# Performance work log

Hardware: AMD Instinct MI355X
Metric: run time of the kernel (lower is better)

The kernel has to match this reference:

```python
import jax, jax.numpy as jnp
from jax import lax
import numpy as np

EPS = 1e-8

def squash(x, axis=-1):
    sq = jnp.sum(x * x, axis=axis, keepdims=True)
    return sq / (1.0 + sq) * x / (jnp.sqrt(sq) + EPS)

def conv1d(x, w, b):
    # x: [B, Cin, L], w: [Cout, Cin, K]
    y = lax.conv_general_dilated(x, w, (1,), 'VALID',
                                 dimension_numbers=('NCH', 'OIH', 'NCH'))
    return y + b[None, :, None]

def setup_inputs() -> dict:
    key = jax.random.key(0)
    ks = jax.random.split(key, 6)
    B = 4096
    x = jax.random.normal(ks[0], (B, 50, 128), dtype=jnp.float32)
    conv1_w = jax.random.normal(ks[1], (50, 128, 9), dtype=jnp.float32) * (1.0 / np.sqrt(128 * 9))
    conv1_b = jnp.zeros((50,), dtype=jnp.float32)
    pconv_w = jax.random.normal(ks[2], (64, 42, 3), dtype=jnp.float32) * (1.0 / np.sqrt(42 * 3))
    pconv_b = jnp.zeros((64,), dtype=jnp.float32)
    W = 0.01 * jax.random.normal(ks[3], (5, 384, 16, 8), dtype=jnp.float32)
    return {"x": x, "conv1_w": conv1_w, "conv1_b": conv1_b,
            "pconv_w": pconv_w, "pconv_b": pconv_b, "W": W}

def reference(x, conv1_w, conv1_b, pconv_w, pconv_b, W):
    B = x.shape[0]
    NUM_ROUTING = 3
    # conv + relu: [B,50,128] -> [B,128,50] -> conv -> [B,50,42] -> permute -> [B,42,50]
    h = conv1d(jnp.transpose(x, (0, 2, 1)), conv1_w, conv1_b)
    h = jnp.transpose(jax.nn.relu(h), (0, 2, 1))  # [B,42,50]
    # primary caps: conv1d -> [B,64,48] -> reshape [B,384,8] -> squash
    p = conv1d(h, pconv_w, pconv_b)
    u = squash(p.reshape(B, -1, 8), axis=-1)  # [B,384,8]
    # u_hat[b,o,c,d] = W[o,c,d,i] * u[b,c,i]
    u_hat = jnp.einsum('ocdi,bci->bocd', W, u)  # [B,5,384,16]
    tu = lax.stop_gradient(u_hat)
    b = jnp.zeros((B, 5, 384, 1), dtype=u_hat.dtype)
    for _ in range(NUM_ROUTING - 1):
        c = jax.nn.softmax(b, axis=1)            # [B,5,384,1]
        s = jnp.sum(c * tu, axis=2)              # [B,5,16]
        v = squash(s)                            # [B,5,16]
        uv = jnp.einsum('bocd,bod->boc', tu, v)[..., None]
        b = b + uv
    c = jax.nn.softmax(b, axis=1)
    s = jnp.sum(c * u_hat, axis=2)
    v = squash(s)  # [B,5,16]
    return v
```

## Files before the change

kernel.cpp:

```cpp
#include <hip/hip_runtime.h>
#include <hip/hip_bf16.h>

typedef unsigned short ushort_t;
typedef _Float16 h2 __attribute__((ext_vector_type(2)));
typedef _Float16 half4_t __attribute__((ext_vector_type(4)));
typedef _Float16 half8_t __attribute__((ext_vector_type(8)));
typedef float f32x4 __attribute__((ext_vector_type(4)));
#define EPSQ 1e-8f

__device__ __forceinline__ float fdot2f(h2 a, h2 b, float c) {
#if __has_builtin(__builtin_amdgcn_fdot2)
  return __builtin_amdgcn_fdot2(a, b, c, false);
#else
  return fmaf((float)a.x, (float)b.x, fmaf((float)a.y, (float)b.y, c));
#endif
}
__device__ __forceinline__ h2 bc_h2(unsigned int v) { return __builtin_bit_cast(h2, v); }
__device__ __forceinline__ unsigned int bc_u32(h2 v) { return __builtin_bit_cast(unsigned int, v); }
__device__ __forceinline__ ushort_t bc_u16(_Float16 v) { return __builtin_bit_cast(ushort_t, v); }


__global__ __launch_bounds__(256) void k0_prep(
    const float* __restrict__ w1, const float* __restrict__ pw,
    const float* __restrict__ Wf,
    _Float16* __restrict__ wc16, _Float16* __restrict__ pwB16,
    _Float16* __restrict__ Wh)
{
  int i = blockIdx.x * 256 + threadIdx.x;
  if (i < 73728) {
    int c  = i / 8192;
    int r  = i % 8192;
    int co = r >> 7;
    int k  = r & 127;
    wc16[i] = (co < 50) ? (_Float16)w1[co*1152 + k*9 + c] : (_Float16)0.f;
  }
  if (i < 10240) {
    int co2 = i / 160, kk = i % 160;
    int k = kk / 48, ci = kk % 48;
    float v = (k < 3 && ci < 42) ? pw[co2*126 + ci*3 + k] : 0.f;
    pwB16[i] = (_Float16)v;
  }
  Wh[i] = (_Float16)Wf[i];
}

__global__ __launch_bounds__(256) void k12_mfma(
    const float* __restrict__ x, const float* __restrict__ b1,
    const float* __restrict__ b2, const _Float16* __restrict__ wc16,
    const _Float16* __restrict__ pwB16, ushort_t* __restrict__ u16)
{
  __shared__ float smem[19728];
  _Float16* xh   = (_Float16*)smem;
  _Float16* hr16 = (_Float16*)smem;
  _Float16* pB   = (_Float16*)smem + 8736;
  float*    pbuf = smem + 9744;

  const int tid   = threadIdx.x;
  const int w     = tid >> 6;
  const int lane  = tid & 63;
  const int lc    = lane & 15;
  const int qd    = lane >> 4;
  const int gbase = blockIdx.x * 3;

  for (int j = tid; j < 4800; j += 256) {
    int g = j / 1600, r = j - g*1600;
    int p = r >> 5, q = r & 31;
    int bb = gbase + g; if (bb > 4095) bb = 4095;
    float4 v = *(const float4*)(x + bb*6400 + p*128 + q*4);
    half4_t hv = {(_Float16)v.x, (_Float16)v.y, (_Float16)v.z, (_Float16)v.w};
    *(half4_t*)(xh + g*6800 + p*136 + q*4) = hv;
  }
  {
    const uint4* wg = (const uint4*)wc16;
    uint4* dst = (uint4*)(xh + 20400);
#pragma unroll
    for (int it = 0; it < 4; ++it) {
      int f = it*256 + tid;
      dst[(f >> 4)*17 + (f & 15)] = wg[f];
    }
  }

  const _Float16* abase[2];
#pragma unroll
  for (int tm = 0; tm < 2; ++tm) {
    int m = 32*w + 16*tm + lc;
    if (m > 125) m = 125;
    int g = m / 42, l = m - g*42;
    abase[tm] = xh + g*6800 + l*136 + qd*8;
  }

  f32x4 acc[2][4];
#pragma unroll
  for (int tm = 0; tm < 2; ++tm)
#pragma unroll
    for (int tn = 0; tn < 4; ++tn)
      acc[tm][tn] = (f32x4){0.f, 0.f, 0.f, 0.f};

  __syncthreads();

  uint4 pf[4];
  for (int c = 0; c < 9; ++c) {
    if (c < 8) {
      const uint4* wg = (const uint4*)wc16 + (c + 1)*1024;
#pragma unroll
      for (int it = 0; it < 4; ++it) pf[it] = wg[it*256 + tid];
    }
    const _Float16* Bb = xh + 20400 + (c & 1)*8704;
    const _Float16* a0 = abase[0] + c*136;
    const _Float16* a1 = abase[1] + c*136;
#pragma unroll
    for (int kk = 0; kk < 128; kk += 32) {
      half8_t av0 = *(const half8_t*)(a0 + kk);
      half8_t av1 = *(const half8_t*)(a1 + kk);
#pragma unroll
      for (int tn = 0; tn < 4; ++tn) {
        half8_t bv = *(const half8_t*)(Bb + (16*tn + lc)*136 + qd*8 + kk);
        acc[0][tn] = __builtin_amdgcn_mfma_f32_16x16x32_f16(av0, bv, acc[0][tn], 0, 0, 0);
        acc[1][tn] = __builtin_amdgcn_mfma_f32_16x16x32_f16(av1, bv, acc[1][tn], 0, 0, 0);
      }
    }
    __syncthreads();
    if (c < 8) {
      uint4* dst = (uint4*)(xh + 20400 + ((c + 1) & 1)*8704);
#pragma unroll
      for (int it = 0; it < 4; ++it) {
        int f = it*256 + tid;
        dst[(f >> 4)*17 + (f & 15)] = pf[it];
      }
      __syncthreads();
    }
  }

  for (int j = tid; j < 4368; j += 256) smem[j] = 0.f;
  {
    const uint4* pg = (const uint4*)pwB16;
    uint4* dst = (uint4*)pB;
    for (int f = tid; f < 1280; f += 256) {
      int row = f / 20, cc = f - row*20;
      dst[row*21 + cc] = pg[f];
    }
  }
  __syncthreads();

#pragma unroll
  for (int tm = 0; tm < 2; ++tm) {
    int mb = 32*w + 16*tm + 4*qd;
#pragma unroll
    for (int tn = 0; tn < 4; ++tn) {
      int co = 16*tn + lc;
      if (co < 50) {
        float bias = b1[co];
#pragma unroll
        for (int r = 0; r < 4; ++r) {
          int m = mb + r;
          if (m < 126) {
            int g = m / 42, l = m - g*42;
            hr16[g*2912 + co*56 + l] = (_Float16)fmaxf(acc[tm][tn][r] + bias, 0.f);
          }
        }
      }
    }
  }
  __syncthreads();

  f32x4 acc2[3][4];
#pragma unroll
  for (int tm = 0; tm < 3; ++tm)
#pragma unroll
    for (int tn = 0; tn < 4; ++tn)
      acc2[tm][tn] = (f32x4){0.f, 0.f, 0.f, 0.f};

#pragma unroll
  for (int kc = 0; kc < 5; ++kc) {
    int kk0 = kc*32 + qd*8;
    int k   = (kk0 >= 144) ? 3 : (kk0 >= 96) ? 2 : (kk0 >= 48) ? 1 : 0;
    int ci0 = kk0 - k*48;
    half8_t bv[4];
#pragma unroll
    for (int tn = 0; tn < 4; ++tn)
      bv[tn] = *(const half8_t*)(pB + (16*tn + lc)*168 + kk0);
#pragma unroll
    for (int tm = 0; tm < 3; ++tm) {
      int T = w + 4*tm; int Tc = (T < 9) ? T : 8;
      int g = Tc/3, l2 = (Tc - g*3)*16 + lc;
      half8_t av = *(const half8_t*)(hr16 + g*2912 + (l2 + k)*56 + ci0);
#pragma unroll
      for (int tn = 0; tn < 4; ++tn)
        acc2[tm][tn] = __builtin_amdgcn_mfma_f32_16x16x32_f16(av, bv[tn], acc2[tm][tn], 0, 0, 0);
    }
  }

#pragma unroll
  for (int tm = 0; tm < 3; ++tm) {
    int T = w + 4*tm;
    if (T < 9) {
      int g = T/3, l2b = (T - g*3)*16;
#pragma unroll
      for (int tn = 0; tn < 4; ++tn) {
        int co2 = 16*tn + lc;
        float bias2 = b2[co2];
#pragma unroll
        for (int r = 0; r < 4; ++r) {
          int l2 = l2b + 4*qd + r;
          pbuf[g*3328 + co2*52 + l2] = acc2[tm][tn][r] + bias2;
        }
      }
    }
  }
  __syncthreads();

  for (int idx = tid; idx < 1152; idx += 256) {
    int g = idx / 384, cap = idx - g*384;
    int bb = gbase + g;
    if (bb < 4096) {
      int co2 = cap / 6, gg = cap - co2*6;
      const float* pp = pbuf + g*3328 + co2*52 + gg*8;
      float4 a0 = *(const float4*)pp;
      float4 a1 = *(const float4*)(pp + 4);
      float sq = a0.x*a0.x + a0.y*a0.y + a0.z*a0.z + a0.w*a0.w
               + a1.x*a1.x + a1.y*a1.y + a1.z*a1.z + a1.w*a1.w;
      float sc = sq / ((1.f + sq) * (sqrtf(sq) + EPSQ));
      h2 p0 = {(_Float16)(a0.x*sc), (_Float16)(a0.y*sc)};
      h2 p1 = {(_Float16)(a0.z*sc), (_Float16)(a0.w*sc)};
      h2 p2 = {(_Float16)(a1.x*sc), (_Float16)(a1.y*sc)};
      h2 p3 = {(_Float16)(a1.z*sc), (_Float16)(a1.w*sc)};
      *(uint4*)(u16 + ((size_t)bb*384 + cap)*8) =
          make_uint4(bc_u32(p0), bc_u32(p1), bc_u32(p2), bc_u32(p3));
    }
  }
}

__global__ __launch_bounds__(384) void k3_route(
    const ushort_t* __restrict__ u16, const _Float16* __restrict__ Wh,
    float* __restrict__ out)
{
  __shared__ __align__(16) ushort_t uh16[80][416];
  __shared__ __align__(16) ushort_t coc16[5][416];
  __shared__ __align__(16) ushort_t svh16[80];
  __shared__ float sv[80];
  __shared__ float ff[5];

  const int t  = threadIdx.x;
  const int b  = blockIdx.x;
  const int q  = t / 96;
  const int jc = t - q*96;
  const int ch = q*104 + jc;

  uint4 uu0 = *(const uint4*)(u16 + ((size_t)b*384 + t)*8);
  h2 ua0[4] = {bc_h2(uu0.x), bc_h2(uu0.y), bc_h2(uu0.z), bc_h2(uu0.w)};

  h2 uhreg[40];
#pragma unroll
  for (int o = 0; o < 5; ++o) {
    const uint4* wp = (const uint4*)(Wh + ((size_t)o*384 + t)*128);
#pragma unroll
    for (int dd = 0; dd < 8; ++dd) {
      uint4 w0 = wp[2*dd], w1 = wp[2*dd + 1];
      float s00 = fdot2f(bc_h2(w0.x), ua0[0], fdot2f(bc_h2(w0.y), ua0[1],
                  fdot2f(bc_h2(w0.z), ua0[2], fdot2f(bc_h2(w0.w), ua0[3], 0.f))));
      float s10 = fdot2f(bc_h2(w1.x), ua0[0], fdot2f(bc_h2(w1.y), ua0[1],
                  fdot2f(bc_h2(w1.z), ua0[2], fdot2f(bc_h2(w1.w), ua0[3], 0.f))));
      _Float16 f00 = (_Float16)s00, f10 = (_Float16)s10;
      uh16[o*16 + 2*dd][ch]     = bc_u16(f00);
      uh16[o*16 + 2*dd + 1][ch] = bc_u16(f10);
      uhreg[o*8 + dd] = (h2){f00, f10};
    }
  }

  float lg[5] = {0.f, 0.f, 0.f, 0.f, 0.f};

  for (int it = 0; it < 3; ++it) {
    {
      float m = fmaxf(fmaxf(fmaxf(lg[0],lg[1]),fmaxf(lg[2],lg[3])),lg[4]);
      float e[5]; float Z = 0.f;
#pragma unroll
      for (int o = 0; o < 5; ++o) { e[o] = __expf(lg[o]-m); Z += e[o]; }
      float inv = 1.f / Z;
#pragma unroll
      for (int o = 0; o < 5; ++o) {
        _Float16 hc = (_Float16)(e[o]*inv);
        coc16[o][ch] = bc_u16(hc);
      }
    }
    __syncthreads();

    if (t < 320) {
      int od = t >> 2, qq = t & 3, o = od >> 4;
      const uint4* ua = (const uint4*)&uh16[od][qq*104];
      const uint4* ca = (const uint4*)&coc16[o][qq*104];
      float sum = 0.f;
#pragma unroll
      for (int j = 0; j < 12; ++j) {
        uint4 uv = ua[j];
        uint4 cv = ca[j];
        sum = fdot2f(bc_h2(uv.x), bc_h2(cv.x), sum);
        sum = fdot2f(bc_h2(uv.y), bc_h2(cv.y), sum);
        sum = fdot2f(bc_h2(uv.z), bc_h2(cv.z), sum);
        sum = fdot2f(bc_h2(uv.w), bc_h2(cv.w), sum);
      }
      sum += __shfl_xor(sum, 1);
      sum += __shfl_xor(sum, 2);
      if (qq == 0) sv[od] = sum;
    }
    __syncthreads();

    if (t < 5) {
      int o = t;
      float sq = 0.f;
#pragma unroll
      for (int d = 0; d < 16; ++d) { float v = sv[o*16+d]; sq = fmaf(v, v, sq); }
      float f = sq / ((1.f + sq) * (sqrtf(sq) + EPSQ));
      ff[o] = f;
      if (it < 2) {
#pragma unroll
        for (int d = 0; d < 16; ++d) {
          _Float16 hf = (_Float16)(sv[o*16+d] * f);
          svh16[o*16+d] = bc_u16(hf);
        }
      }
    }
    __syncthreads();

    if (it == 2) {
      if (t < 80) {
        out[(size_t)b*80 + t] = sv[t] * ff[t >> 4];
      }
    } else {
#pragma unroll
      for (int o = 0; o < 5; ++o) {
        uint4 s0 = *(const uint4*)&svh16[o*16];
        uint4 s1 = *(const uint4*)&svh16[o*16 + 8];
        float dv = 0.f;
        dv = fdot2f(uhreg[o*8+0], bc_h2(s0.x), dv);
        dv = fdot2f(uhreg[o*8+1], bc_h2(s0.y), dv);
        dv = fdot2f(uhreg[o*8+2], bc_h2(s0.z), dv);
        dv = fdot2f(uhreg[o*8+3], bc_h2(s0.w), dv);
        dv = fdot2f(uhreg[o*8+4], bc_h2(s1.x), dv);
        dv = fdot2f(uhreg[o*8+5], bc_h2(s1.y), dv);
        dv = fdot2f(uhreg[o*8+6], bc_h2(s1.z), dv);
        dv = fdot2f(uhreg[o*8+7], bc_h2(s1.w), dv);
        lg[o] += dv;
      }
    }
  }
}

extern "C" void kernel_launch(void* const* d_in, const int* in_sizes, int n_in,
                              void* d_out, int out_size, void* d_ws, size_t ws_size,
                              hipStream_t stream) {
  const float* x  = (const float*)d_in[0];
  const float* w1 = (const float*)d_in[1];
  const float* b1 = (const float*)d_in[2];
  const float* pw = (const float*)d_in[3];
  const float* b2 = (const float*)d_in[4];
  const float* Wf = (const float*)d_in[5];
  float* out = (float*)d_out;
  char* ws = (char*)d_ws;

  _Float16* wc16  = (_Float16*)(ws);
  _Float16* pwB16 = (_Float16*)(ws + 147456);
  _Float16* Wh    = (_Float16*)(ws + 167936);
  ushort_t* u16   = (ushort_t*)(ws + 659456);

  k0_prep<<<960, 256, 0, stream>>>(w1, pw, Wf, wc16, pwB16, Wh);
  k12_mfma<<<1366, 256, 0, stream>>>(x, b1, b2, wc16, pwB16, u16);
  k3_route<<<4096, 384, 0, stream>>>(u16, Wh, out);
}
```

Before: 517.8 us.

## Replace shared-memory routing reduction with wave DPP reductions and coalesced W layout

The routing kernel no longer stages u_hat and coupling coefficients in a large shared array. Each thread keeps its u_hat in registers, multiplies by the softmax coefficients, and reduces across the wave with DPP row shifts and xor shuffles. Per-wave partials are written to a small shared buffer, and the squash norm is computed with shuffles instead of a single-thread loop. The W tensor is also reordered in the prep kernel so that consecutive threads load contiguous 16-byte chunks, which coalesces the global reads. Together these cut LDS footprint and barriers, but add many cross-lane reduction ops (16 values times 5 capsules per iteration).

```diff
diff --git a/kernel.cpp b/kernel.cpp
--- a/kernel.cpp
+++ b/kernel.cpp
@@ -19,12 +19,18 @@
 __device__ __forceinline__ unsigned int bc_u32(h2 v) { return __builtin_bit_cast(unsigned int, v); }
 __device__ __forceinline__ ushort_t bc_u16(_Float16 v) { return __builtin_bit_cast(ushort_t, v); }
 
+template<int CTRL>
+__device__ __forceinline__ float dpp_addf(float x) {
+  int y = __builtin_amdgcn_update_dpp(0, __builtin_bit_cast(int, x), CTRL, 0xf, 0xf, false);
+  return x + __builtin_bit_cast(float, y);
+}
+
 
 __global__ __launch_bounds__(256) void k0_prep(
     const float* __restrict__ w1, const float* __restrict__ pw,
     const float* __restrict__ Wf,
     _Float16* __restrict__ wc16, _Float16* __restrict__ pwB16,
-    _Float16* __restrict__ Wh)
+    _Float16* __restrict__ Whs)
 {
   int i = blockIdx.x * 256 + threadIdx.x;
   if (i < 73728) {
@@ -40,7 +46,15 @@
     float v = (k < 3 && ci < 42) ? pw[co2*126 + ci*3 + k] : 0.f;
     pwB16[i] = (_Float16)v;
   }
-  Wh[i] = (_Float16)Wf[i];
+  {
+    int i8 = i & 7;
+    int r  = i >> 3;
+    int d  = r & 15;
+    int rc = r >> 4;
+    int c  = rc % 384;
+    int o  = rc / 384;
+    Whs[(((o*16 + d)*384) + c)*8 + i8] = (_Float16)Wf[i];
+  }
 }
 
 __global__ __launch_bounds__(256) void k12_mfma(
@@ -229,102 +243,96 @@
   }
 }
 
-__global__ __launch_bounds__(384) void k3_route(
-    const ushort_t* __restrict__ u16, const _Float16* __restrict__ Wh,
+__global__ __launch_bounds__(384, 4) void k3_route(
+    const ushort_t* __restrict__ u16, const _Float16* __restrict__ Whs,
     float* __restrict__ out)
 {
-  __shared__ __align__(16) ushort_t uh16[80][416];
-  __shared__ __align__(16) ushort_t coc16[5][416];
+  __shared__ __align__(16) float part[6][80];
   __shared__ __align__(16) ushort_t svh16[80];
-  __shared__ float sv[80];
-  __shared__ float ff[5];
-
-  const int t  = threadIdx.x;
-  const int b  = blockIdx.x;
-  const int q  = t / 96;
-  const int jc = t - q*96;
-  const int ch = q*104 + jc;
+
+  const int t    = threadIdx.x;
+  const int b    = blockIdx.x;
+  const int w    = t >> 6;
+  const int lane = t & 63;
 
   uint4 uu0 = *(const uint4*)(u16 + ((size_t)b*384 + t)*8);
   h2 ua0[4] = {bc_h2(uu0.x), bc_h2(uu0.y), bc_h2(uu0.z), bc_h2(uu0.w)};
 
   h2 uhreg[40];
+  const uint4* wb = (const uint4*)Whs;
 #pragma unroll
   for (int o = 0; o < 5; ++o) {
-    const uint4* wp = (const uint4*)(Wh + ((size_t)o*384 + t)*128);
+    const uint4* wp = wb + (size_t)(o*16)*384 + t;
 #pragma unroll
     for (int dd = 0; dd < 8; ++dd) {
-      uint4 w0 = wp[2*dd], w1 = wp[2*dd + 1];
+      uint4 w0 = wp[(size_t)(2*dd)*384];
+      uint4 w1 = wp[(size_t)(2*dd + 1)*384];
       float s00 = fdot2f(bc_h2(w0.x), ua0[0], fdot2f(bc_h2(w0.y), ua0[1],
                   fdot2f(bc_h2(w0.z), ua0[2], fdot2f(bc_h2(w0.w), ua0[3], 0.f))));
       float s10 = fdot2f(bc_h2(w1.x), ua0[0], fdot2f(bc_h2(w1.y), ua0[1],
                   fdot2f(bc_h2(w1.z), ua0[2], fdot2f(bc_h2(w1.w), ua0[3], 0.f))));
-      _Float16 f00 = (_Float16)s00, f10 = (_Float16)s10;
-      uh16[o*16 + 2*dd][ch]     = bc_u16(f00);
-      uh16[o*16 + 2*dd + 1][ch] = bc_u16(f10);
-      uhreg[o*8 + dd] = (h2){f00, f10};
+      uhreg[o*8 + dd] = (h2){(_Float16)s00, (_Float16)s10};
     }
   }
 
   float lg[5] = {0.f, 0.f, 0.f, 0.f, 0.f};
 
   for (int it = 0; it < 3; ++it) {
+    float co[5];
     {
       float m = fmaxf(fmaxf(fmaxf(lg[0],lg[1]),fmaxf(lg[2],lg[3])),lg[4]);
-      float e[5]; float Z = 0.f;
-#pragma unroll
-      for (int o = 0; o < 5; ++o) { e[o] = __expf(lg[o]-m); Z += e[o]; }
+      float Z = 0.f;
+#pragma unroll
+      for (int o = 0; o < 5; ++o) { co[o] = __expf(lg[o]-m); Z += co[o]; }
       float inv = 1.f / Z;
 #pragma unroll
-      for (int o = 0; o < 5; ++o) {
-        _Float16 hc = (_Float16)(e[o]*inv);
-        coc16[o][ch] = bc_u16(hc);
+      for (int o = 0; o < 5; ++o) co[o] *= inv;
+    }
+
+#pragma unroll
+    for (int o = 0; o < 5; ++o) {
+      float pr[16];
+#pragma unroll
+      for (int dd = 0; dd < 8; ++dd) {
+        h2 uh = uhreg[o*8 + dd];
+        pr[2*dd]     = co[o] * (float)uh.x;
+        pr[2*dd + 1] = co[o] * (float)uh.y;
+      }
+#pragma unroll
+      for (int j = 0; j < 16; ++j) {
+        float v = pr[j];
+        v = dpp_addf<0x121>(v);
+        v = dpp_addf<0x122>(v);
+        v = dpp_addf<0x124>(v);
+        v = dpp_addf<0x128>(v);
+        v += __shfl_xor(v, 16);
+        v += __shfl_xor(v, 32);
+        pr[j] = v;
+      }
+#pragma unroll
+      for (int j = 0; j < 8; ++j) {
+        if (lane == o*8 + j) {
+          *(float2*)&part[w][o*16 + 2*j] = make_float2(pr[2*j], pr[2*j + 1]);
+        }
       }
     }
     __syncthreads();
 
-    if (t < 320) {
-      int od = t >> 2, qq = t & 3, o = od >> 4;
-      const uint4* ua = (const uint4*)&uh16[od][qq*104];
-      const uint4* ca = (const uint4*)&coc16[o][qq*104];
-      float sum = 0.f;
-#pragma unroll
-      for (int j = 0; j < 12; ++j) {
-        uint4 uv = ua[j];
-        uint4 cv = ca[j];
-        sum = fdot2f(bc_h2(uv.x), bc_h2(cv.x), sum);
-        sum = fdot2f(bc_h2(uv.y), bc_h2(cv.y), sum);
-        sum = fdot2f(bc_h2(uv.z), bc_h2(cv.z), sum);
-        sum = fdot2f(bc_h2(uv.w), bc_h2(cv.w), sum);
-      }
-      sum += __shfl_xor(sum, 1);
-      sum += __shfl_xor(sum, 2);
-      if (qq == 0) sv[od] = sum;
+    if (t < 80) {
+      float s = part[0][t] + part[1][t] + part[2][t]
+              + part[3][t] + part[4][t] + part[5][t];
+      float sq = s * s;
+      sq += __shfl_xor(sq, 1);
+      sq += __shfl_xor(sq, 2);
+      sq += __shfl_xor(sq, 4);
+      sq += __shfl_xor(sq, 8);
+      float f = sq / ((1.f + sq) * (sqrtf(sq) + EPSQ));
+      if (it == 2) out[(size_t)b*80 + t] = s * f;
+      else         svh16[t] = bc_u16((_Float16)(s * f));
     }
     __syncthreads();
 
-    if (t < 5) {
-      int o = t;
-      float sq = 0.f;
-#pragma unroll
-      for (int d = 0; d < 16; ++d) { float v = sv[o*16+d]; sq = fmaf(v, v, sq); }
-      float f = sq / ((1.f + sq) * (sqrtf(sq) + EPSQ));
-      ff[o] = f;
-      if (it < 2) {
-#pragma unroll
-        for (int d = 0; d < 16; ++d) {
-          _Float16 hf = (_Float16)(sv[o*16+d] * f);
-          svh16[o*16+d] = bc_u16(hf);
-        }
-      }
-    }
-    __syncthreads();
-
-    if (it == 2) {
-      if (t < 80) {
-        out[(size_t)b*80 + t] = sv[t] * ff[t >> 4];
-      }
-    } else {
+    if (it < 2) {
 #pragma unroll
       for (int o = 0; o < 5; ++o) {
         uint4 s0 = *(const uint4*)&svh16[o*16];
@@ -358,10 +366,10 @@
 
   _Float16* wc16  = (_Float16*)(ws);
   _Float16* pwB16 = (_Float16*)(ws + 147456);
-  _Float16* Wh    = (_Float16*)(ws + 167936);
+  _Float16* Whs   = (_Float16*)(ws + 167936);
   ushort_t* u16   = (ushort_t*)(ws + 659456);
 
-  k0_prep<<<960, 256, 0, stream>>>(w1, pw, Wf, wc16, pwB16, Wh);
+  k0_prep<<<960, 256, 0, stream>>>(w1, pw, Wf, wc16, pwB16, Whs);
   k12_mfma<<<1366, 256, 0, stream>>>(x, b1, b2, wc16, pwB16, u16);
-  k3_route<<<4096, 384, 0, stream>>>(u16, Wh, out);
-}
+  k3_route<<<4096, 384, 0, stream>>>(u16, Whs, out);
+}
```

Result: slower. 768.1 us (+48.3%).
